# Optimization experiments

Hardware: AMD Instinct MI355X
Metric: run time of the kernel (lower is better)

## Reference

```python
import jax, jax.numpy as jnp
import numpy as np

T, D_IN, R, D_OUT = 4096, 512, 4096, 512
LEAK = 0.9
SCALE_IN = 1.0
DENSITY = 0.5
SPECTRAL_RADIUS = 0.9


def setup_inputs() -> dict:
    key = jax.random.key(0)
    ks = jax.random.split(key, 7)
    x = jax.random.normal(ks[0], (T, D_IN), dtype=jnp.float32)
    Win_w = jax.random.uniform(ks[1], (R, D_IN), minval=-SCALE_IN, maxval=SCALE_IN, dtype=jnp.float32)
    Win_b = jax.random.uniform(ks[2], (R,), minval=-SCALE_IN, maxval=SCALE_IN, dtype=jnp.float32)
    # Wres: sparse uniform matrix rescaled to target spectral radius.
    Wres_w = jax.random.uniform(ks[3], (R, R), minval=-1.0, maxval=1.0, dtype=jnp.float32)
    mask = jax.random.bernoulli(ks[4], DENSITY, (R, R)).astype(jnp.float32)
    Wres_w = Wres_w * mask
    # spectral radius of a dense-ish random uniform matrix ~ sqrt(R*density*var), var(U[-1,1])=1/3
    approx_rho = np.sqrt(R * DENSITY / 3.0)
    Wres_w = Wres_w * (SPECTRAL_RADIUS / approx_rho)
    Nint = R + D_IN
    lim = 1.0 / np.sqrt(Nint)
    Wout_w = jax.random.uniform(ks[5], (D_OUT, Nint), minval=-lim, maxval=lim, dtype=jnp.float32)
    Wout_b = jax.random.uniform(ks[6], (D_OUT,), minval=-lim, maxval=lim, dtype=jnp.float32)
    return {"x": x, "Win_w": Win_w, "Win_b": Win_b, "Wres_w": Wres_w,
            "Wout_w": Wout_w, "Wout_b": Wout_b}


def reference(x, Win_w, Win_b, Wres_w, Wout_w, Wout_b):
    # Precompute the input projection for all timesteps (one GEMM).
    u = x @ Win_w.T + Win_b                       # (T, R)
    s0 = jnp.tanh(u[0])                           # (R,)

    def step(s, ui):
        xi = jnp.tanh(ui + Wres_w @ s)
        s_new = (1.0 - LEAK) * s + LEAK * xi      # leaky integration
        return s_new, s_new

    _, rest = jax.lax.scan(step, s0, u[1:])       # (T-1, R)
    states = jnp.concatenate([s0[None, :], rest], axis=0)  # (T, R)
    xall = jnp.concatenate([x, states], axis=1)   # (T, D_IN + R)
    yout = xall @ Wout_w.T + Wout_b               # (T, D_OUT)
    return yout
```

## Files before the change

### kernel.cpp

```cpp
#include <hip/hip_runtime.h>

#define T_STEPS 4096
#define DIN     512
#define R_DIM   4096
#define DOUT    512
#define NINT    (R_DIM + DIN)
#define NBLK    256
#define NTHR    512
#define NUNIT   2048
#define LEAKF   0.9f

typedef float f32x4 __attribute__((ext_vector_type(4)));
typedef unsigned int u32;
typedef u32 u32x2 __attribute__((ext_vector_type(2)));

__device__ __forceinline__ float fast_tanh(float x)
{
    float e = __builtin_amdgcn_exp2f(x * 2.885390081777927f);
    return 1.0f - 2.0f * __builtin_amdgcn_rcpf(1.0f + e);
}

__device__ __forceinline__ u32 f2bf(float f)
{
    u32 u = __float_as_uint(f);
    return (u + 0x7FFFu + ((u >> 16) & 1u)) >> 16;
}

__device__ __forceinline__ float wave_reduce2(float a0, float a1, int lane)
{
    a0 += __shfl_xor(a0, 1);
    a1 += __shfl_xor(a1, 1);
    float b = (lane & 1) ? a1 : a0;
    b += __shfl_xor(b, 2);
    b += __shfl_xor(b, 4);
    b += __shfl_xor(b, 8);
    b += __shfl_xor(b, 16);
    b += __shfl_xor(b, 32);
    return b;
}

__global__ __launch_bounds__(NTHR, 2) void esn_fused(
    const float* __restrict__ x,
    const float* __restrict__ Win_w,
    const float* __restrict__ Win_b,
    const float* __restrict__ Wres,
    const float* __restrict__ Wout_w,
    const float* __restrict__ Wout_b,
    float* __restrict__ y,
    u32x2* __restrict__ comm)
{
    const int tid  = threadIdx.x;
    const int wave = tid >> 6;
    const int lane = tid & 63;
    const int bid  = blockIdx.x;
    const int row_e = (bid << 4) + (wave << 1);

    __shared__ float s_lds[2][R_DIM];
    __shared__ float wout_lds[2 * NINT];

    {
        const float* wsrc = Wout_w + (size_t)(bid << 1) * NINT;
        for (int idx = tid; idx < 2 * NINT; idx += NTHR)
            wout_lds[idx] = wsrc[idx];
    }
    float wb = 0.f;
    if (wave < 2 && lane == 0) wb = Wout_b[(bid << 1) + wave];

    f32x4 w[2][16];
    {
        const float* wp = Wres + (size_t)row_e * R_DIM + (lane << 2);
#pragma unroll
        for (int r = 0; r < 2; ++r)
#pragma unroll
            for (int c = 0; c < 16; ++c)
                w[r][c] = *(const f32x4*)(wp + (size_t)r * R_DIM + (c << 8));
    }
    f32x4 win[2][2];
    {
        const float* ip = Win_w + (size_t)row_e * DIN + (lane << 2);
#pragma unroll
        for (int r = 0; r < 2; ++r)
#pragma unroll
            for (int c = 0; c < 2; ++c)
                win[r][c] = *(const f32x4*)(ip + (size_t)r * DIN + (c << 8));
    }
    const float bias_e = Win_b[row_e];
    const float bias_o = Win_b[row_e + 1];
    float s_old_e = 0.f, s_old_o = 0.f;

    float a0, a1;

#define PROJ(xrow)                                                        \
    {                                                                     \
        f32x4 xv0 = *(const f32x4*)((xrow) + (lane << 2));                \
        f32x4 xv1 = *(const f32x4*)((xrow) + 256 + (lane << 2));          \
        a0 = 0.f; a1 = 0.f;                                               \
        _Pragma("unroll")                                                 \
        for (int q = 0; q < 4; ++q) {                                     \
            a0 += win[0][0][q] * xv0[q] + win[0][1][q] * xv1[q];          \
            a1 += win[1][0][q] * xv0[q] + win[1][1][q] * xv1[q];          \
        }                                                                 \
    }

#define PUBLISH(sn_e, sn_o, tagv, bufsel)                                 \
    if (lane == 0) {                                                      \
        u32x2 pkt;                                                        \
        pkt.x = f2bf(sn_e) | (f2bf(sn_o) << 16);                          \
        pkt.y = (u32)(tagv);                                              \
        u32x2* dst = comm + ((bufsel) * NUNIT) + (bid << 3) + wave;       \
        asm volatile("global_store_dwordx2 %0, %1, off sc0 sc1"           \
                     :: "v"(dst), "v"(pkt) : "memory");                   \
    }

    {
        PROJ(x);
        float b = wave_reduce2(a0, a1, lane);
        float se = __shfl(b, 0) + bias_e;
        float so = __shfl(b, 1) + bias_o;
        float sn_e = fast_tanh(se);
        float sn_o = fast_tanh(so);
        s_old_e = sn_e; s_old_o = sn_o;
        PUBLISH(sn_e, sn_o, 1u, 0);
    }
    PROJ(x + DIN);

    for (int i = 1; i <= T_STEPS; ++i) {
        const int p = (i - 1) & 1;

        {
            const u32x2* src = comm + (p * NUNIT) + (tid << 2);
            const u32 tag = (u32)i;
            u32x2 q0, q1, q2, q3;
            for (;;) {
                asm volatile("global_load_dwordx2 %0, %4, off sc0 sc1\n\t"
                             "global_load_dwordx2 %1, %5, off sc0 sc1\n\t"
                             "global_load_dwordx2 %2, %6, off sc0 sc1\n\t"
                             "global_load_dwordx2 %3, %7, off sc0 sc1\n\t"
                             "s_waitcnt vmcnt(0)"
                             : "=&v"(q0), "=&v"(q1), "=&v"(q2), "=&v"(q3)
                             : "v"(src), "v"(src + 1), "v"(src + 2), "v"(src + 3)
                             : "memory");
                u32 ok = (q0.y == tag) & (q1.y == tag) &
                         (q2.y == tag) & (q3.y == tag);
                if (ok) break;
                __builtin_amdgcn_s_sleep(1);
            }
            f32x4 lo, hi;
            lo[0] = __uint_as_float((q0.x & 0xFFFFu) << 16);
            lo[1] = __uint_as_float(q0.x & 0xFFFF0000u);
            lo[2] = __uint_as_float((q1.x & 0xFFFFu) << 16);
            lo[3] = __uint_as_float(q1.x & 0xFFFF0000u);
            hi[0] = __uint_as_float((q2.x & 0xFFFFu) << 16);
            hi[1] = __uint_as_float(q2.x & 0xFFFF0000u);
            hi[2] = __uint_as_float((q3.x & 0xFFFFu) << 16);
            hi[3] = __uint_as_float(q3.x & 0xFFFF0000u);
            *(f32x4*)&s_lds[p][tid << 3] = lo;
            *(f32x4*)&s_lds[p][(tid << 3) + 4] = hi;
        }
        __syncthreads();

        if (i < T_STEPS) {
            const f32x4* s4 = (const f32x4*)&s_lds[p][0] + lane;
#pragma unroll
            for (int c = 0; c < 16; ++c) {
                f32x4 sv = s4[c << 6];
#pragma unroll
                for (int q = 0; q < 4; ++q) {
                    a0 += w[0][c][q] * sv[q];
                    a1 += w[1][c][q] * sv[q];
                }
            }
            float b = wave_reduce2(a0, a1, lane);
            float se = __shfl(b, 0) + bias_e;
            float so = __shfl(b, 1) + bias_o;
            float sn_e = (1.f - LEAKF) * s_old_e + LEAKF * fast_tanh(se);
            float sn_o = (1.f - LEAKF) * s_old_o + LEAKF * fast_tanh(so);
            s_old_e = sn_e; s_old_o = sn_o;
            PUBLISH(sn_e, sn_o, (u32)(i + 1), i & 1);
        }

        if (wave < 2) {
            const float* wrow = wout_lds + wave * NINT;
            float acc = 0.f;
            {
                const float* xr = x + (size_t)(i - 1) * DIN + (lane << 3);
                f32x4 xa = *(const f32x4*)xr;
                f32x4 xb = *(const f32x4*)(xr + 4);
                const f32x4* wr4 = (const f32x4*)wrow + (lane << 1);
                f32x4 wa = wr4[0], wbv = wr4[1];
#pragma unroll
                for (int q = 0; q < 4; ++q)
                    acc += xa[q] * wa[q] + xb[q] * wbv[q];
            }
            {
                const f32x4* s4 = (const f32x4*)&s_lds[p][0] + lane;
                const f32x4* wr4 = (const f32x4*)(wrow + DIN) + lane;
#pragma unroll
                for (int c = 0; c < 16; ++c) {
                    f32x4 sv = s4[c << 6];
                    f32x4 wv = wr4[c << 6];
#pragma unroll
                    for (int q = 0; q < 4; ++q)
                        acc += sv[q] * wv[q];
                }
            }
            acc += __shfl_xor(acc, 1);
            acc += __shfl_xor(acc, 2);
            acc += __shfl_xor(acc, 4);
            acc += __shfl_xor(acc, 8);
            acc += __shfl_xor(acc, 16);
            acc += __shfl_xor(acc, 32);
            if (lane == 0)
                y[(size_t)(i - 1) * DOUT + (bid << 1) + wave] = acc + wb;
        }

        if (i + 1 < T_STEPS) PROJ(x + (size_t)(i + 1) * DIN);
    }
#undef PROJ
#undef PUBLISH
}

extern "C" void kernel_launch(void* const* d_in, const int* in_sizes, int n_in,
                              void* d_out, int out_size, void* d_ws, size_t ws_size,
                              hipStream_t stream) {
    const float* x      = (const float*)d_in[0];
    const float* Win_w  = (const float*)d_in[1];
    const float* Win_b  = (const float*)d_in[2];
    const float* Wres_w = (const float*)d_in[3];
    const float* Wout_w = (const float*)d_in[4];
    const float* Wout_b = (const float*)d_in[5];
    float* yp = (float*)d_out;

    u32x2* comm = (u32x2*)d_ws;

    hipMemsetAsync(d_ws, 0, 2 * NUNIT * sizeof(u32x2), stream);

    void* args[] = { (void*)&x, (void*)&Win_w, (void*)&Win_b, (void*)&Wres_w,
                     (void*)&Wout_w, (void*)&Wout_b, (void*)&yp, (void*)&comm };
    hipLaunchCooperativeKernel((void*)esn_fused, dim3(NBLK), dim3(NTHR),
                               args, 0, stream);
}
```

Baseline: 10.34 ms.

## Spread readout over six waves and poll state chunks independently

Measured after the change: 12.71 ms. +22.9%, slower.

```diff
diff --git a/kernel.cpp b/kernel.cpp
--- a/kernel.cpp
+++ b/kernel.cpp
@@ -13,6 +13,7 @@
 typedef float f32x4 __attribute__((ext_vector_type(4)));
 typedef unsigned int u32;
 typedef u32 u32x2 __attribute__((ext_vector_type(2)));
+typedef u32 u32x4 __attribute__((ext_vector_type(4)));
 
 __device__ __forceinline__ float fast_tanh(float x)
 {
@@ -25,6 +26,8 @@
     u32 u = __float_as_uint(f);
     return (u + 0x7FFFu + ((u >> 16) & 1u)) >> 16;
 }
+__device__ __forceinline__ float bfLO(u32 u) { return __uint_as_float(u << 16); }
+__device__ __forceinline__ float bfHI(u32 u) { return __uint_as_float(u & 0xFFFF0000u); }
 
 __device__ __forceinline__ float wave_reduce2(float a0, float a1, int lane)
 {
@@ -57,14 +60,15 @@
 
     __shared__ float s_lds[2][R_DIM];
     __shared__ float wout_lds[2 * NINT];
+    __shared__ float red2[2][6][2];
 
     {
         const float* wsrc = Wout_w + (size_t)(bid << 1) * NINT;
         for (int idx = tid; idx < 2 * NINT; idx += NTHR)
             wout_lds[idx] = wsrc[idx];
     }
-    float wb = 0.f;
-    if (wave < 2 && lane == 0) wb = Wout_b[(bid << 1) + wave];
+    float wbf = 0.f;
+    if (wave == 2 && lane < 2) wbf = Wout_b[(bid << 1) + lane];
 
     f32x4 w[2][16];
     {
@@ -128,48 +132,57 @@
         const int p = (i - 1) & 1;
 
         {
-            const u32x2* src = comm + (p * NUNIT) + (tid << 2);
+            const u32x4* src = (const u32x4*)(comm + p * NUNIT) + (tid << 1);
             const u32 tag = (u32)i;
-            u32x2 q0, q1, q2, q3;
+            u32x4 qa, qb;
+            u32 pend = 3u;
             for (;;) {
-                asm volatile("global_load_dwordx2 %0, %4, off sc0 sc1\n\t"
-                             "global_load_dwordx2 %1, %5, off sc0 sc1\n\t"
-                             "global_load_dwordx2 %2, %6, off sc0 sc1\n\t"
-                             "global_load_dwordx2 %3, %7, off sc0 sc1\n\t"
-                             "s_waitcnt vmcnt(0)"
-                             : "=&v"(q0), "=&v"(q1), "=&v"(q2), "=&v"(q3)
-                             : "v"(src), "v"(src + 1), "v"(src + 2), "v"(src + 3)
-                             : "memory");
-                u32 ok = (q0.y == tag) & (q1.y == tag) &
-                         (q2.y == tag) & (q3.y == tag);
-                if (ok) break;
+                if (pend & 1u)
+                    asm volatile("global_load_dwordx4 %0, %1, off sc0 sc1"
+                                 : "=&v"(qa) : "v"(src) : "memory");
+                if (pend & 2u)
+                    asm volatile("global_load_dwordx4 %0, %1, off sc0 sc1"
+                                 : "=&v"(qb) : "v"(src + 1) : "memory");
+                asm volatile("s_waitcnt vmcnt(0)" ::: "memory");
+                if ((pend & 1u) && (qa.y == tag) && (qa.w == tag)) {
+                    f32x4 v;
+                    v[0] = bfLO(qa.x); v[1] = bfHI(qa.x);
+                    v[2] = bfLO(qa.z); v[3] = bfHI(qa.z);
+                    *(f32x4*)&s_lds[p][tid << 3] = v;
+                    pend &= ~1u;
+                }
+                if ((pend & 2u) && (qb.y == tag) && (qb.w == tag)) {
+                    f32x4 v;
+                    v[0] = bfLO(qb.x); v[1] = bfHI(qb.x);
+                    v[2] = bfLO(qb.z); v[3] = bfHI(qb.z);
+                    *(f32x4*)&s_lds[p][(tid << 3) + 4] = v;
+                    pend &= ~2u;
+                }
+                if (!pend) break;
                 __builtin_amdgcn_s_sleep(1);
             }
-            f32x4 lo, hi;
-            lo[0] = __uint_as_float((q0.x & 0xFFFFu) << 16);
-            lo[1] = __uint_as_float(q0.x & 0xFFFF0000u);
-            lo[2] = __uint_as_float((q1.x & 0xFFFFu) << 16);
-            lo[3] = __uint_as_float(q1.x & 0xFFFF0000u);
-            hi[0] = __uint_as_float((q2.x & 0xFFFFu) << 16);
-            hi[1] = __uint_as_float(q2.x & 0xFFFF0000u);
-            hi[2] = __uint_as_float((q3.x & 0xFFFFu) << 16);
-            hi[3] = __uint_as_float(q3.x & 0xFFFF0000u);
-            *(f32x4*)&s_lds[p][tid << 3] = lo;
-            *(f32x4*)&s_lds[p][(tid << 3) + 4] = hi;
         }
         __syncthreads();
+
+        if (i >= 2 && wave == 2 && lane < 2) {
+            const int rp = i & 1;
+            float s = red2[rp][0][lane] + red2[rp][1][lane] + red2[rp][2][lane]
+                    + red2[rp][3][lane] + red2[rp][4][lane] + red2[rp][5][lane];
+            y[(size_t)(i - 2) * DOUT + (bid << 1) + lane] = s + wbf;
+        }
 
         if (i < T_STEPS) {
             const f32x4* s4 = (const f32x4*)&s_lds[p][0] + lane;
+            float a0b = 0.f, a1b = 0.f;
 #pragma unroll
             for (int c = 0; c < 16; ++c) {
                 f32x4 sv = s4[c << 6];
-#pragma unroll
-                for (int q = 0; q < 4; ++q) {
-                    a0 += w[0][c][q] * sv[q];
-                    a1 += w[1][c][q] * sv[q];
-                }
+                a0  += w[0][c][0] * sv[0] + w[0][c][1] * sv[1];
+                a0b += w[0][c][2] * sv[2] + w[0][c][3] * sv[3];
+                a1  += w[1][c][0] * sv[0] + w[1][c][1] * sv[1];
+                a1b += w[1][c][2] * sv[2] + w[1][c][3] * sv[3];
             }
+            a0 += a0b; a1 += a1b;
             float b = wave_reduce2(a0, a1, lane);
             float se = __shfl(b, 0) + bias_e;
             float so = __shfl(b, 1) + bias_o;
@@ -179,42 +192,29 @@
             PUBLISH(sn_e, sn_o, (u32)(i + 1), i & 1);
         }
 
-        if (wave < 2) {
-            const float* wrow = wout_lds + wave * NINT;
-            float acc = 0.f;
-            {
-                const float* xr = x + (size_t)(i - 1) * DIN + (lane << 3);
-                f32x4 xa = *(const f32x4*)xr;
-                f32x4 xb = *(const f32x4*)(xr + 4);
-                const f32x4* wr4 = (const f32x4*)wrow + (lane << 1);
-                f32x4 wa = wr4[0], wbv = wr4[1];
-#pragma unroll
-                for (int q = 0; q < 4; ++q)
-                    acc += xa[q] * wa[q] + xb[q] * wbv[q];
+        if (wave >= 2) {
+            const int w6 = wave - 2;
+            const float* xrow = x + (size_t)(i - 1) * DIN;
+            float y0 = 0.f, y1 = 0.f;
+#pragma unroll
+            for (int k = 0; k < 12; ++k) {
+                int col = w6 * 768 + (k << 6) + lane;
+                float v = (col < DIN) ? xrow[col] : s_lds[p][col - DIN];
+                y0 += wout_lds[col] * v;
+                y1 += wout_lds[NINT + col] * v;
             }
-            {
-                const f32x4* s4 = (const f32x4*)&s_lds[p][0] + lane;
-                const f32x4* wr4 = (const f32x4*)(wrow + DIN) + lane;
-#pragma unroll
-                for (int c = 0; c < 16; ++c) {
-                    f32x4 sv = s4[c << 6];
-                    f32x4 wv = wr4[c << 6];
-#pragma unroll
-                    for (int q = 0; q < 4; ++q)
-                        acc += sv[q] * wv[q];
-                }
-            }
-            acc += __shfl_xor(acc, 1);
-            acc += __shfl_xor(acc, 2);
-            acc += __shfl_xor(acc, 4);
-            acc += __shfl_xor(acc, 8);
-            acc += __shfl_xor(acc, 16);
-            acc += __shfl_xor(acc, 32);
-            if (lane == 0)
-                y[(size_t)(i - 1) * DOUT + (bid << 1) + wave] = acc + wb;
+            float b = wave_reduce2(y0, y1, lane);
+            if (lane < 2) red2[(i - 1) & 1][w6][lane] = b;
         }
 
         if (i + 1 < T_STEPS) PROJ(x + (size_t)(i + 1) * DIN);
+    }
+
+    __syncthreads();
+    if (wave == 2 && lane < 2) {
+        float s = red2[1][0][lane] + red2[1][1][lane] + red2[1][2][lane]
+                + red2[1][3][lane] + red2[1][4][lane] + red2[1][5][lane];
+        y[(size_t)(T_STEPS - 1) * DOUT + (bid << 1) + lane] = s + wbf;
     }
 #undef PROJ
 #undef PUBLISH
```
